# Optimization experiments

Measured on AMD Instinct MI355X. Metric: run time of the kernel, lower is better.

## Reference

```python
import jax, jax.numpy as jnp
import numpy as np

NUM_OBJ_CLS = 151


def setup_inputs() -> dict:
    key = jax.random.key(0)
    ks = jax.random.split(key, 12)
    N, H, E, U, P, R = 6144, 512, 49152, 2048, 4096, 51
    return {
        "edge_ctx": jax.random.normal(ks[0], (N, H), jnp.float32),
        "union_features": jax.random.normal(ks[1], (E, U), jnp.float32),
        "W_post_emb": jax.random.normal(ks[2], (H, 2 * H), jnp.float32) * (H ** -0.5),
        "b_post_emb": jnp.zeros((2 * H,), jnp.float32),
        "W_post_cat": jax.random.normal(ks[3], (2 * H, P), jnp.float32) * ((2 * H) ** -0.5),
        "b_post_cat": jnp.zeros((P,), jnp.float32),
        "W_up": jax.random.normal(ks[4], (U, P), jnp.float32) * (U ** -0.5),
        "b_up": jnp.zeros((P,), jnp.float32),
        "W_rel": jax.random.normal(ks[5], (P, R), jnp.float32) * (P ** -0.5),
        "b_rel": jnp.zeros((R,), jnp.float32),
        "freq_table": jax.random.normal(ks[6], (NUM_OBJ_CLS * NUM_OBJ_CLS, R), jnp.float32),
        "obj_preds": jax.random.randint(ks[7], (N,), 0, NUM_OBJ_CLS, jnp.int64),
        "pair_idx": jax.random.randint(ks[8], (E, 2), 0, N, jnp.int64),
    }


def reference(edge_ctx, union_features, W_post_emb, b_post_emb, W_post_cat,
              b_post_cat, W_up, b_up, W_rel, b_rel, freq_table,
              obj_preds, pair_idx):
    N, H = edge_ctx.shape
    # post_emb -> split into head/tail representations [N, H] each
    edge_rep = (edge_ctx @ W_post_emb + b_post_emb).reshape(N, 2, H)
    head_rep, tail_rep = edge_rep[:, 0], edge_rep[:, 1]
    # gather per-pair head/tail reps and concat -> [E, 2H]
    prod_rep = jnp.concatenate(
        (head_rep[pair_idx[:, 0]], tail_rep[pair_idx[:, 1]]), axis=-1)
    prod_rep = prod_rep @ W_post_cat + b_post_cat            # [E, P]
    # union feature up-projection (union_single_not_match) and gating multiply
    prod_rep = prod_rep * (union_features @ W_up + b_up)     # [E, P]
    rel_dists = prod_rep @ W_rel + b_rel                     # [E, R]
    # frequency-bias lookup indexed by (head_class, tail_class)
    bias_idx = obj_preds[pair_idx[:, 0]] * NUM_OBJ_CLS + obj_preds[pair_idx[:, 1]]
    rel_dists = rel_dists + freq_table[bias_idx]
    return rel_dists
```

## Files before the change

### kernel.cpp

```cpp
#include <hip/hip_runtime.h>

typedef unsigned short u16;
typedef __attribute__((ext_vector_type(4))) float f32x4;
typedef __attribute__((ext_vector_type(4))) u16 u16x4;
typedef __attribute__((ext_vector_type(8))) u16 u16x8;
typedef __attribute__((ext_vector_type(8))) short short8;

__device__ __forceinline__ u16 f2bf(float f) {
  unsigned int u = __builtin_bit_cast(unsigned int, f);
  u += 0x7FFFu + ((u >> 16) & 1u);
  return (u16)(u >> 16);
}
__device__ __forceinline__ float bf2f(u16 b) {
  unsigned int u = ((unsigned int)b) << 16;
  return __builtin_bit_cast(float, u);
}

__device__ __forceinline__ void gld16(const void* g, void* l) {
  __builtin_amdgcn_global_load_lds(
      (const __attribute__((address_space(1))) unsigned int*)g,
      (__attribute__((address_space(3))) unsigned int*)l, 16, 0, 0);
}

template <int N>
__device__ __forceinline__ void boundary() {
  asm volatile("s_waitcnt vmcnt(%0)" ::"n"(N) : "memory");
  __builtin_amdgcn_s_barrier();
  asm volatile("" ::: "memory");
  __builtin_amdgcn_sched_barrier(0);
}


__global__ __launch_bounds__(256) void cvt_f32_bf16(const float* __restrict__ s,
                                                    u16* __restrict__ d, long n4) {
  long stride = (long)gridDim.x * 256;
  for (long i = (long)blockIdx.x * 256 + threadIdx.x; i < n4; i += stride) {
    f32x4 v = *(const f32x4*)(s + i * 4);
    u16x4 o = {f2bf(v.x), f2bf(v.y), f2bf(v.z), f2bf(v.w)};
    *(u16x4*)(d + i * 4) = o;
  }
}

__global__ __launch_bounds__(256) void transpose_f32_bf16(const float* __restrict__ src,
                                                          u16* __restrict__ dst,
                                                          int R, int C, int CP) {
  __shared__ float tile[32][33];
  int r0 = blockIdx.x * 32, c0 = blockIdx.y * 32;
  int tx = threadIdx.x & 31, ty = threadIdx.x >> 5;
#pragma unroll
  for (int i = 0; i < 32; i += 8) {
    int r = r0 + ty + i, c = c0 + tx;
    tile[ty + i][tx] = (r < R && c < C) ? src[(size_t)r * C + c] : 0.f;
  }
  __syncthreads();
#pragma unroll
  for (int i = 0; i < 32; i += 8) {
    int c = c0 + ty + i, r = r0 + tx;
    if (c < CP && r < R) dst[(size_t)c * R + r] = f2bf(tile[tx][ty + i]);
  }
}


template <int NROW>
__device__ __forceinline__ void stage_direct(const u16* __restrict__ src, int ld,
                                             int kcol0, u16* lds, int tid) {
#pragma unroll
  for (int it = 0; it < NROW / 32; ++it) {
    int idx = it * 256 + tid;
    int row = idx >> 3, c = idx & 7;
    int cc = c ^ (row & 7);
    gld16(src + (size_t)row * ld + kcol0 + cc * 8, (char*)lds + idx * 16);
  }
}

template <int MI>
__device__ __forceinline__ void mma_step(const char* As, const char* Bs, int arow0,
                                         int brow0, int lane, f32x4 acc[MI][4]) {
  int r = lane & 15, q = lane >> 4;
#pragma unroll
  for (int ks = 0; ks < 2; ++ks) {
    short8 a[MI], b[4];
#pragma unroll
    for (int i = 0; i < MI; ++i) {
      int row = arow0 + i * 16 + r;
      a[i] = *(const short8*)(As + row * 128 + ((((ks << 2) + q) ^ (row & 7)) << 4));
    }
#pragma unroll
    for (int j = 0; j < 4; ++j) {
      int row = brow0 + j * 16 + r;
      b[j] = *(const short8*)(Bs + row * 128 + ((((ks << 2) + q) ^ (row & 7)) << 4));
    }
#pragma unroll
    for (int i = 0; i < MI; ++i)
#pragma unroll
      for (int j = 0; j < 4; ++j)
        acc[i][j] = __builtin_amdgcn_mfma_f32_16x16x32_bf16(a[i], b[j], acc[i][j], 0, 0, 0);
  }
}


__global__ __launch_bounds__(256) void gemm1(const u16* __restrict__ ec,
                                             const u16* __restrict__ WpeT,
                                             const float* __restrict__ bpe,
                                             u16* __restrict__ head,
                                             u16* __restrict__ tail) {
  __shared__ __align__(16) u16 As[128 * 64];
  __shared__ __align__(16) u16 Bs[128 * 64];
  int tid = threadIdx.x, lane = tid & 63, wave = tid >> 6;
  int wrow = wave >> 1, wcol = wave & 1;
  int m0 = blockIdx.x * 128, n0 = blockIdx.y * 128;
  f32x4 z = {0.f, 0.f, 0.f, 0.f};
  f32x4 acc[4][4];
#pragma unroll
  for (int i = 0; i < 4; ++i)
#pragma unroll
    for (int j = 0; j < 4; ++j) acc[i][j] = z;

  for (int kb = 0; kb < 8; ++kb) {
    stage_direct<128>(ec + (size_t)m0 * 512, 512, kb * 64, As, tid);
    stage_direct<128>(WpeT + (size_t)n0 * 512, 512, kb * 64, Bs, tid);
    __syncthreads();
    mma_step<4>((const char*)As, (const char*)Bs, wrow * 64, wcol * 64, lane, acc);
    __syncthreads();
  }
  int r = lane & 15, q = lane >> 4;
#pragma unroll
  for (int i = 0; i < 4; ++i) {
    int e = m0 + wrow * 64 + i * 16 + q * 4;
#pragma unroll
    for (int j = 0; j < 4; ++j) {
      int c = n0 + wcol * 64 + j * 16 + r;
      float bb = bpe[c];
#pragma unroll
      for (int g = 0; g < 4; ++g) {
        float v = acc[i][j][g] + bb;
        if (c < 512) head[(size_t)(e + g) * 512 + c] = f2bf(v);
        else         tail[(size_t)(e + g) * 512 + (c - 512)] = f2bf(v);
      }
    }
  }
}


__global__ __launch_bounds__(256) void gemm_hp(const u16* __restrict__ A,
                                               const u16* __restrict__ BT,
                                               u16* __restrict__ P) {
  __shared__ __align__(16) u16 As[128 * 64];
  __shared__ __align__(16) u16 Bs[128 * 64];
  int tid = threadIdx.x, lane = tid & 63, wave = tid >> 6;
  int wrow = wave >> 1, wcol = wave & 1;
  int m0 = blockIdx.x * 128, n0 = blockIdx.y * 128;
  f32x4 z = {0.f, 0.f, 0.f, 0.f};
  f32x4 acc[4][4];
#pragma unroll
  for (int i = 0; i < 4; ++i)
#pragma unroll
    for (int j = 0; j < 4; ++j) acc[i][j] = z;

  for (int kb = 0; kb < 8; ++kb) {
    stage_direct<128>(A + (size_t)m0 * 512, 512, kb * 64, As, tid);
    stage_direct<128>(BT + (size_t)n0 * 512, 512, kb * 64, Bs, tid);
    __syncthreads();
    mma_step<4>((const char*)As, (const char*)Bs, wrow * 64, wcol * 64, lane, acc);
    __syncthreads();
  }
  int r = lane & 15, q = lane >> 4;
#pragma unroll
  for (int i = 0; i < 4; ++i) {
    int e = m0 + wrow * 64 + i * 16 + q * 4;
#pragma unroll
    for (int j = 0; j < 4; ++j) {
      int c = n0 + wcol * 64 + j * 16 + r;
#pragma unroll
      for (int g = 0; g < 4; ++g)
        P[(size_t)(e + g) * 4096 + c] = f2bf(acc[i][j][g]);
    }
  }
}


__global__ __launch_bounds__(512, 2) void gemm_union_fuse4(
    const u16* __restrict__ U, const u16* __restrict__ WupT,
    const float* __restrict__ bup, const float* __restrict__ bpc,
    const u16* __restrict__ Hp, const u16* __restrict__ Tp,
    const int* __restrict__ pair, const u16* __restrict__ WrelT,
    float* __restrict__ Pp) {
  extern __shared__ __align__(16) u16 lds[];
  const int tid = threadIdx.x, lane = tid & 63, wave = tid >> 6;
  const int wm = wave >> 2, wn = wave & 3;
  const int r = lane & 15, q = lane >> 4;

  int bid = blockIdx.x;
  int swz = (bid & 7) * 384 + (bid >> 3);
  int m0 = (swz >> 4) * 256, n0 = (swz & 15) * 256;

  const u16* Apanel = U + (size_t)m0 * 2048;
  const u16* Bpanel = WupT + (size_t)n0 * 2048;

  f32x4 acc[8][4];
  f32x4 z = {0.f, 0.f, 0.f, 0.f};
#pragma unroll
  for (int i = 0; i < 8; ++i)
#pragma unroll
    for (int j = 0; j < 4; ++j) acc[i][j] = z;

  auto STAGE = [&](int buf, int mat, int kt, int kh) {
    const u16* src = mat ? Bpanel : Apanel;
#pragma unroll
    for (int it = 0; it < 2; ++it) {
      int id = it * 512 + tid;
      int row = id >> 2, c4 = id & 3;
      gld16(src + (size_t)row * 2048 + kt * 64 + kh * 32 + ((c4 ^ ((row >> 1) & 3)) << 3),
            lds + ((((buf << 1) | mat) << 1 | kh) << 13) + id * 8);
    }
  };
  auto LDA = [&](int buf, int kh, int mi) -> short8 {
    int row = wm * 128 + mi * 16 + r;
    return *(const short8*)(lds + (((buf << 1) << 1 | kh) << 13) + row * 32 +
                            ((q ^ ((r >> 1) & 3)) << 3));
  };
  auto LDB = [&](int buf, int kh, int nj) -> short8 {
    int row = wn * 64 + nj * 16 + r;
    return *(const short8*)(lds + ((((buf << 1) | 1) << 1 | kh) << 13) + row * 32 +
                            ((q ^ ((r >> 1) & 3)) << 3));
  };

  STAGE(0, 0, 0, 0);
  STAGE(0, 1, 0, 0);
  STAGE(0, 0, 0, 1);
  STAGE(0, 1, 0, 1);
  boundary<4>();

  short8 a[4], b[4];
  const int NT = 32;
  for (int t = 0; t < NT; ++t) {
    int cur = t & 1, nxt = cur ^ 1;
    bool more = (t < NT - 1);

#pragma unroll
    for (int nj = 0; nj < 4; ++nj) b[nj] = LDB(cur, 0, nj);
#pragma unroll
    for (int mi = 0; mi < 4; ++mi) a[mi] = LDA(cur, 0, mi);
    if (more) STAGE(nxt, 0, t + 1, 0);
    __builtin_amdgcn_s_setprio(1);
#pragma unroll
    for (int mi = 0; mi < 4; ++mi)
#pragma unroll
      for (int nj = 0; nj < 4; ++nj)
        acc[mi][nj] = __builtin_amdgcn_mfma_f32_16x16x32_bf16(a[mi], b[nj], acc[mi][nj], 0, 0, 0);
    __builtin_amdgcn_s_setprio(0);

#pragma unroll
    for (int mi = 0; mi < 4; ++mi) a[mi] = LDA(cur, 0, mi + 4);
    if (more) STAGE(nxt, 1, t + 1, 0);
    __builtin_amdgcn_s_setprio(1);
#pragma unroll
    for (int mi = 0; mi < 4; ++mi)
#pragma unroll
      for (int nj = 0; nj < 4; ++nj)
        acc[mi + 4][nj] = __builtin_amdgcn_mfma_f32_16x16x32_bf16(a[mi], b[nj], acc[mi + 4][nj], 0, 0, 0);
    __builtin_amdgcn_s_setprio(0);

    if (t == NT - 1) boundary<0>(); else boundary<4>();

#pragma unroll
    for (int nj = 0; nj < 4; ++nj) b[nj] = LDB(cur, 1, nj);
#pragma unroll
    for (int mi = 0; mi < 4; ++mi) a[mi] = LDA(cur, 1, mi);
    if (more) STAGE(nxt, 0, t + 1, 1);
    __builtin_amdgcn_s_setprio(1);
#pragma unroll
    for (int mi = 0; mi < 4; ++mi)
#pragma unroll
      for (int nj = 0; nj < 4; ++nj)
        acc[mi][nj] = __builtin_amdgcn_mfma_f32_16x16x32_bf16(a[mi], b[nj], acc[mi][nj], 0, 0, 0);
    __builtin_amdgcn_s_setprio(0);

#pragma unroll
    for (int mi = 0; mi < 4; ++mi) a[mi] = LDA(cur, 1, mi + 4);
    if (more) STAGE(nxt, 1, t + 1, 1);
    __builtin_amdgcn_s_setprio(1);
#pragma unroll
    for (int mi = 0; mi < 4; ++mi)
#pragma unroll
      for (int nj = 0; nj < 4; ++nj)
        acc[mi + 4][nj] = __builtin_amdgcn_mfma_f32_16x16x32_bf16(a[mi], b[nj], acc[mi + 4][nj], 0, 0, 0);
    __builtin_amdgcn_s_setprio(0);

    if (more) boundary<4>();
  }

  __syncthreads();

  u16* Uw = lds + (wave << 13);
#pragma unroll
  for (int mi = 0; mi < 8; ++mi) {
#pragma unroll
    for (int nj = 0; nj < 4; ++nj) {
      int col = nj * 16 + r;
      float bb = bup[n0 + wn * 64 + col];
#pragma unroll
      for (int g = 0; g < 4; ++g) {
        int rw = mi * 16 + q * 4 + g;
        int byte_off = rw * 128 + ((((col >> 3) ^ (rw & 7)) << 4)) + (col & 7) * 2;
        *(u16*)((char*)Uw + byte_off) = f2bf(acc[mi][nj][g] + bb);
      }
    }
  }
  asm volatile("s_waitcnt lgkmcnt(0)" ::: "memory");
  __builtin_amdgcn_sched_barrier(0);

  int c0 = n0 + wn * 64;
#pragma unroll
  for (int rr = 0; rr < 2; ++rr) {
    int lr = lane * 2 + rr;
    int e = m0 + wm * 128 + lr;
    int h = pair[2 * e], tt = pair[2 * e + 1];
    const u16* hp = Hp + (size_t)h * 4096 + c0;
    const u16* tp = Tp + (size_t)tt * 4096 + c0;
#pragma unroll
    for (int ch = 0; ch < 8; ++ch) {
      u16x8 hv = *(const u16x8*)(hp + ch * 8);
      u16x8 tv = *(const u16x8*)(tp + ch * 8);
      u16* slot = (u16*)((char*)Uw + lr * 128 + ((ch ^ (lr & 7)) << 4));
      u16x8 uv = *(u16x8*)slot;
      u16x8 o;
#pragma unroll
      for (int k = 0; k < 8; ++k) {
        float p = bf2f(hv[k]) + bf2f(tv[k]) + bpc[c0 + ch * 8 + k];
        o[k] = f2bf(bf2f(uv[k]) * p);
      }
      *(u16x8*)slot = o;
    }
  }
  __syncthreads();

  f32x4 acc2[2][4];
#pragma unroll
  for (int i = 0; i < 2; ++i)
#pragma unroll
    for (int j = 0; j < 4; ++j) acc2[i][j] = z;

#pragma unroll
  for (int ks = 0; ks < 8; ++ks) {
    int wn_k = ks >> 1;
    int cb = (ks & 1) * 4;
    short8 a2[2], b2[4];
#pragma unroll
    for (int i = 0; i < 2; ++i) {
      int rr2 = wave * 32 + i * 16 + r;
      int reg = ((rr2 >> 7) << 2) | wn_k;
      int lr2 = rr2 & 127;
      int ch = cb + q;
      a2[i] = *(const short8*)((char*)lds + reg * 16384 + lr2 * 128 +
                               ((ch ^ (lr2 & 7)) << 4));
    }
#pragma unroll
    for (int j = 0; j < 4; ++j)
      b2[j] = *(const short8*)(WrelT + (size_t)(j * 16 + r) * 4096 + n0 + ks * 32 + q * 8);
#pragma unroll
    for (int i = 0; i < 2; ++i)
#pragma unroll
      for (int j = 0; j < 4; ++j)
        acc2[i][j] = __builtin_amdgcn_mfma_f32_16x16x32_bf16(a2[i], b2[j], acc2[i][j], 0, 0, 0);
  }

  int nt = n0 >> 8;
#pragma unroll
  for (int i = 0; i < 2; ++i) {
#pragma unroll
    for (int j = 0; j < 4; ++j) {
      int col = j * 16 + r;
#pragma unroll
      for (int g = 0; g < 4; ++g) {
        int e = m0 + wave * 32 + i * 16 + q * 4 + g;
        Pp[((size_t)nt * 49152 + e) * 64 + col] = acc2[i][j][g];
      }
    }
  }
}


__global__ __launch_bounds__(256) void reduce_out(const float* __restrict__ Pp,
                                                  const float* __restrict__ brel,
                                                  const float* __restrict__ freq,
                                                  const int* __restrict__ obj,
                                                  const int* __restrict__ pair,
                                                  float* __restrict__ out) {
  int e = blockIdx.x * 4 + (threadIdx.x >> 6);
  int c = threadIdx.x & 63;
  const float* p = Pp + (size_t)e * 64 + c;
  float s = 0.f;
#pragma unroll
  for (int nt = 0; nt < 16; ++nt) s += p[(size_t)nt * 49152 * 64];
  if (c < 51) {
    int bidx = obj[pair[2 * e]] * 151 + obj[pair[2 * e + 1]];
    out[(size_t)e * 51 + c] = s + brel[c] + freq[(size_t)bidx * 51 + c];
  }
}


extern "C" void kernel_launch(void* const* d_in, const int* in_sizes, int n_in,
                              void* d_out, int out_size, void* d_ws, size_t ws_size,
                              hipStream_t stream) {
  const float* edge_ctx = (const float*)d_in[0];
  const float* unionf   = (const float*)d_in[1];
  const float* Wpe      = (const float*)d_in[2];
  const float* bpe      = (const float*)d_in[3];
  const float* Wpc      = (const float*)d_in[4];
  const float* bpc      = (const float*)d_in[5];
  const float* Wup      = (const float*)d_in[6];
  const float* bup      = (const float*)d_in[7];
  const float* Wrel     = (const float*)d_in[8];
  const float* brel     = (const float*)d_in[9];
  const float* freq     = (const float*)d_in[10];
  const int*   obj      = (const int*)d_in[11];
  const int*   pair     = (const int*)d_in[12];
  float* out = (float*)d_out;

  u16* ws = (u16*)d_ws;
  float* Pp    = (float*)ws;
  u16* ub      = ws + 201326592;
  u16* ec      = ws + 301989888;
  u16* head    = ws + 305135616;
  u16* tail    = ws + 308281344;
  u16* WpeT    = ws + 311427072;
  u16* WpcTopT = ws + 311951360;
  u16* WpcBotT = ws + 314048512;
  u16* WupT    = ws + 316145664;
  u16* WrelT   = ws + 324534272;
  u16* Hp      = ws + 324796416;
  u16* Tp      = ws + 349962240;

  cvt_f32_bf16<<<768, 256, 0, stream>>>(edge_ctx, ec, 786432);
  cvt_f32_bf16<<<4096, 256, 0, stream>>>(unionf, ub, 25165824);
  transpose_f32_bf16<<<dim3(16, 32), 256, 0, stream>>>(Wpe, WpeT, 512, 1024, 1024);
  transpose_f32_bf16<<<dim3(16, 128), 256, 0, stream>>>(Wpc, WpcTopT, 512, 4096, 4096);
  transpose_f32_bf16<<<dim3(16, 128), 256, 0, stream>>>(Wpc + (size_t)512 * 4096, WpcBotT, 512, 4096, 4096);
  transpose_f32_bf16<<<dim3(64, 128), 256, 0, stream>>>(Wup, WupT, 2048, 4096, 4096);
  transpose_f32_bf16<<<dim3(128, 2), 256, 0, stream>>>(Wrel, WrelT, 4096, 51, 64);

  gemm1<<<dim3(48, 8), 256, 0, stream>>>(ec, WpeT, bpe, head, tail);
  gemm_hp<<<dim3(48, 32), 256, 0, stream>>>(head, WpcTopT, Hp);
  gemm_hp<<<dim3(48, 32), 256, 0, stream>>>(tail, WpcBotT, Tp);
  gemm_union_fuse4<<<3072, 512, 131072, stream>>>(ub, WupT, bup, bpc, Hp, Tp, pair, WrelT, Pp);
  reduce_out<<<12288, 256, 0, stream>>>(Pp, brel, freq, obj, pair, out);
}
```

Baseline: 1.298 ms.

## Restructure GEMM main loop into 8-phase schedule with barriers between LDS reads and MFMA

Unrolls the K loop by two tiles and restages loads so each sub-tile half is prefetched further ahead, with an s_barrier plus lgkmcnt wait between every LDS fragment read and its MFMA block. Separate A-fragment registers for the two row halves let loads and MFMAs interleave across waves. The aim is a finer-grained, ping-pong style overlap of global-to-LDS staging with matrix math. The cost is many more workgroup barriers per iteration, which can stall waves.

```diff
diff --git a/kernel.cpp b/kernel.cpp
--- a/kernel.cpp
+++ b/kernel.cpp
@@ -225,70 +225,109 @@
                             ((q ^ ((r >> 1) & 3)) << 3));
   };
 
-  STAGE(0, 0, 0, 0);
-  STAGE(0, 1, 0, 0);
-  STAGE(0, 0, 0, 1);
-  STAGE(0, 1, 0, 1);
+#define MID_BAR()                                                     \
+  do {                                                                \
+    __builtin_amdgcn_sched_barrier(0);                                \
+    __builtin_amdgcn_s_barrier();                                     \
+    asm volatile("s_waitcnt lgkmcnt(0)" ::: "memory");                \
+    __builtin_amdgcn_sched_barrier(0);                                \
+  } while (0)
+
+  short8 a0[4], a1[4], b[4];
+
+  auto MMA0 = [&]() {
+    __builtin_amdgcn_s_setprio(1);
+#pragma unroll
+    for (int mi = 0; mi < 4; ++mi)
+#pragma unroll
+      for (int nj = 0; nj < 4; ++nj)
+        acc[mi][nj] = __builtin_amdgcn_mfma_f32_16x16x32_bf16(a0[mi], b[nj], acc[mi][nj], 0, 0, 0);
+    __builtin_amdgcn_s_setprio(0);
+  };
+  auto MMA1 = [&]() {
+    __builtin_amdgcn_s_setprio(1);
+#pragma unroll
+    for (int mi = 0; mi < 4; ++mi)
+#pragma unroll
+      for (int nj = 0; nj < 4; ++nj)
+        acc[mi + 4][nj] = __builtin_amdgcn_mfma_f32_16x16x32_bf16(a1[mi], b[nj], acc[mi + 4][nj], 0, 0, 0);
+    __builtin_amdgcn_s_setprio(0);
+  };
+
+  STAGE(0, 0, 0, 0); STAGE(0, 1, 0, 0);
+  STAGE(0, 0, 0, 1); STAGE(0, 1, 0, 1);
+  STAGE(1, 0, 1, 0); STAGE(1, 1, 1, 0);
   boundary<4>();
 
-  short8 a[4], b[4];
   const int NT = 32;
-  for (int t = 0; t < NT; ++t) {
-    int cur = t & 1, nxt = cur ^ 1;
-    bool more = (t < NT - 1);
-
-#pragma unroll
-    for (int nj = 0; nj < 4; ++nj) b[nj] = LDB(cur, 0, nj);
-#pragma unroll
-    for (int mi = 0; mi < 4; ++mi) a[mi] = LDA(cur, 0, mi);
-    if (more) STAGE(nxt, 0, t + 1, 0);
-    __builtin_amdgcn_s_setprio(1);
-#pragma unroll
-    for (int mi = 0; mi < 4; ++mi)
-#pragma unroll
-      for (int nj = 0; nj < 4; ++nj)
-        acc[mi][nj] = __builtin_amdgcn_mfma_f32_16x16x32_bf16(a[mi], b[nj], acc[mi][nj], 0, 0, 0);
-    __builtin_amdgcn_s_setprio(0);
-
-#pragma unroll
-    for (int mi = 0; mi < 4; ++mi) a[mi] = LDA(cur, 0, mi + 4);
-    if (more) STAGE(nxt, 1, t + 1, 0);
-    __builtin_amdgcn_s_setprio(1);
-#pragma unroll
-    for (int mi = 0; mi < 4; ++mi)
-#pragma unroll
-      for (int nj = 0; nj < 4; ++nj)
-        acc[mi + 4][nj] = __builtin_amdgcn_mfma_f32_16x16x32_bf16(a[mi], b[nj], acc[mi + 4][nj], 0, 0, 0);
-    __builtin_amdgcn_s_setprio(0);
-
-    if (t == NT - 1) boundary<0>(); else boundary<4>();
-
-#pragma unroll
-    for (int nj = 0; nj < 4; ++nj) b[nj] = LDB(cur, 1, nj);
-#pragma unroll
-    for (int mi = 0; mi < 4; ++mi) a[mi] = LDA(cur, 1, mi);
-    if (more) STAGE(nxt, 0, t + 1, 1);
-    __builtin_amdgcn_s_setprio(1);
-#pragma unroll
-    for (int mi = 0; mi < 4; ++mi)
-#pragma unroll
-      for (int nj = 0; nj < 4; ++nj)
-        acc[mi][nj] = __builtin_amdgcn_mfma_f32_16x16x32_bf16(a[mi], b[nj], acc[mi][nj], 0, 0, 0);
-    __builtin_amdgcn_s_setprio(0);
-
-#pragma unroll
-    for (int mi = 0; mi < 4; ++mi) a[mi] = LDA(cur, 1, mi + 4);
-    if (more) STAGE(nxt, 1, t + 1, 1);
-    __builtin_amdgcn_s_setprio(1);
-#pragma unroll
-    for (int mi = 0; mi < 4; ++mi)
-#pragma unroll
-      for (int nj = 0; nj < 4; ++nj)
-        acc[mi + 4][nj] = __builtin_amdgcn_mfma_f32_16x16x32_bf16(a[mi], b[nj], acc[mi + 4][nj], 0, 0, 0);
-    __builtin_amdgcn_s_setprio(0);
-
+  for (int t = 0; t < NT; t += 2) {
+    bool more = (t + 2 < NT);
+
+#pragma unroll
+    for (int nj = 0; nj < 4; ++nj) b[nj] = LDB(0, 0, nj);
+#pragma unroll
+    for (int mi = 0; mi < 4; ++mi) a0[mi] = LDA(0, 0, mi);
+    STAGE(1, 0, t + 1, 1);
+    MID_BAR();
+    MMA0();
+    __builtin_amdgcn_s_barrier();
+
+#pragma unroll
+    for (int mi = 0; mi < 4; ++mi) a1[mi] = LDA(0, 0, mi + 4);
+    STAGE(1, 1, t + 1, 1);
+    MID_BAR();
+    MMA1();
+    __builtin_amdgcn_s_barrier();
+
+#pragma unroll
+    for (int nj = 0; nj < 4; ++nj) b[nj] = LDB(0, 1, nj);
+#pragma unroll
+    for (int mi = 0; mi < 4; ++mi) a0[mi] = LDA(0, 1, mi);
+    if (more) STAGE(0, 0, t + 2, 0);
+    MID_BAR();
+    MMA0();
+    __builtin_amdgcn_s_barrier();
+
+#pragma unroll
+    for (int mi = 0; mi < 4; ++mi) a1[mi] = LDA(0, 1, mi + 4);
+    if (more) STAGE(0, 1, t + 2, 0);
+    MID_BAR();
+    MMA1();
+    if (more) boundary<4>(); else boundary<0>();
+
+#pragma unroll
+    for (int nj = 0; nj < 4; ++nj) b[nj] = LDB(1, 0, nj);
+#pragma unroll
+    for (int mi = 0; mi < 4; ++mi) a0[mi] = LDA(1, 0, mi);
+    if (more) STAGE(0, 0, t + 2, 1);
+    MID_BAR();
+    MMA0();
+    __builtin_amdgcn_s_barrier();
+
+#pragma unroll
+    for (int mi = 0; mi < 4; ++mi) a1[mi] = LDA(1, 0, mi + 4);
+    if (more) STAGE(0, 1, t + 2, 1);
+    MID_BAR();
+    MMA1();
+    __builtin_amdgcn_s_barrier();
+
+#pragma unroll
+    for (int nj = 0; nj < 4; ++nj) b[nj] = LDB(1, 1, nj);
+#pragma unroll
+    for (int mi = 0; mi < 4; ++mi) a0[mi] = LDA(1, 1, mi);
+    if (more) STAGE(1, 0, t + 3, 0);
+    MID_BAR();
+    MMA0();
+    __builtin_amdgcn_s_barrier();
+
+#pragma unroll
+    for (int mi = 0; mi < 4; ++mi) a1[mi] = LDA(1, 1, mi + 4);
+    if (more) STAGE(1, 1, t + 3, 0);
+    MID_BAR();
+    MMA1();
     if (more) boundary<4>();
   }
+#undef MID_BAR
 
   __syncthreads();
 
```

Result: no change. 1.323 ms (+2.0%).
